# Kernel optimization log

Measured on AMD Instinct MI355X. Metric: run time of the kernel, lower is better.

## Reference

```python
import jax, jax.numpy as jnp
import numpy as np

B, N, D = 4096, 7, 512  # batch, sample_num, embed dim


def _l2_normalize(x, eps=1e-12):
    # torch F.normalize: x / max(||x||, eps)
    n = jnp.sqrt(jnp.sum(x * x, axis=-1, keepdims=True))
    return x / jnp.maximum(n, eps)


def setup_inputs() -> dict:
    key = jax.random.key(0)
    ks = jax.random.split(key, 6)
    return {
        "query_mean": jax.random.normal(ks[0], (B, D), jnp.float32),
        "query_logsigma": jax.random.normal(ks[1], (B, D), jnp.float32),
        "target_mean": jax.random.normal(ks[2], (B, D), jnp.float32),
        "target_logsigma": jax.random.normal(ks[3], (B, D), jnp.float32),
        "eps_q": jax.random.normal(ks[4], (B, N, D), jnp.float32),
        "eps_k": jax.random.normal(ks[5], (B, N, D), jnp.float32),
    }


def reference(query_mean, query_logsigma, target_mean, target_logsigma, eps_q, eps_k):
    temperature = 1.0
    qm = _l2_normalize(query_mean)               # [B, D]
    tm = _l2_normalize(target_mean)              # [B, D]
    # sample_gaussian_tensors: mu + eps * exp(logsigma), per-sample noise
    q = qm[:, None, :] + eps_q * jnp.exp(query_logsigma)[:, None, :]   # [B, N, D]
    k = tm[:, None, :] + eps_k * jnp.exp(target_logsigma)[:, None, :]  # [B, N, D]
    n = q.shape[1]
    # monto_carlo_estimation: score[i,j] = mean over N*N pairwise dots
    # = (sum_n q[i]) . (sum_m k[j]) / (N*N)  -- fused single gemm instead of B*B tiny matmuls
    score = jnp.einsum('id,jd->ij', q.sum(axis=1), k.sum(axis=1)) / (n * n)  # [B, B]
    logits = score / temperature
    # cross_entropy with labels = arange(B), reduction='mean'
    logp = jax.nn.log_softmax(logits, axis=-1)
    loss = -jnp.mean(jnp.diagonal(logp))
    return loss
```

## Files before the change

kernel.cpp:

```cpp
#include <hip/hip_runtime.h>

#define NBATCH 4096
#define NSAMP  7
#define DIM    512
#define NCB    16

typedef float floatx4 __attribute__((ext_vector_type(4)));
typedef short short8  __attribute__((ext_vector_type(8)));

__device__ static __forceinline__ void load16_lds(const void* g, void* l) {
  __builtin_amdgcn_global_load_lds(
      (const __attribute__((address_space(1))) unsigned int*)g,
      (__attribute__((address_space(3))) unsigned int*)l, 16, 0, 0);
}

__device__ static __forceinline__ unsigned int f2bf_rne(float f) {
  union { float f; unsigned int u; } v; v.f = f;
  unsigned int u = v.u;
  u += 0x7FFFu + ((u >> 16) & 1u);
  return u >> 16;
}

__global__ __launch_bounds__(256, 4) void prep_kernel(
    const float* __restrict__ qm, const float* __restrict__ qls, const float* __restrict__ eq,
    const float* __restrict__ tm, const float* __restrict__ tls, const float* __restrict__ ek,
    unsigned short* __restrict__ outA, unsigned short* __restrict__ outB)
{
  const int wv   = threadIdx.x >> 6;
  const int lane = threadIdx.x & 63;
  const int gid  = blockIdx.x * 4 + wv;
  const int side = gid >> 12;
  const int row  = gid & (NBATCH - 1);

  const float* mean = side ? tm  : qm;
  const float* ls   = side ? tls : qls;
  const float* eps  = side ? ek  : eq;
  unsigned short* out = side ? outB : outA;

  const float4* mean4 = (const float4*)(mean + (size_t)row * DIM);
  const float4* ls4   = (const float4*)(ls   + (size_t)row * DIM);
  const float4* eps4  = (const float4*)(eps  + (size_t)row * (NSAMP * DIM));

  const float4 m0 = mean4[lane];
  const float4 m1 = mean4[64 + lane];
  const float4 l0 = ls4[lane];
  const float4 l1 = ls4[64 + lane];
  float4 e0[NSAMP], e1[NSAMP];
  #pragma unroll
  for (int n = 0; n < NSAMP; ++n) {
    e0[n] = eps4[n * (DIM / 4) + lane];
    e1[n] = eps4[n * (DIM / 4) + 64 + lane];
  }

  float ss = m0.x * m0.x + m0.y * m0.y + m0.z * m0.z + m0.w * m0.w
           + m1.x * m1.x + m1.y * m1.y + m1.z * m1.z + m1.w * m1.w;
  #pragma unroll
  for (int off = 1; off < 64; off <<= 1) ss += __shfl_xor(ss, off);
  const float rnorm = 1.0f / fmaxf(sqrtf(ss), 1e-12f);

  float s00 = 0.f, s01 = 0.f, s02 = 0.f, s03 = 0.f;
  float s10 = 0.f, s11 = 0.f, s12 = 0.f, s13 = 0.f;
  #pragma unroll
  for (int n = 0; n < NSAMP; ++n) {
    s00 += e0[n].x; s01 += e0[n].y; s02 += e0[n].z; s03 += e0[n].w;
    s10 += e1[n].x; s11 += e1[n].y; s12 += e1[n].z; s13 += e1[n].w;
  }

  const float inv = 1.0f / (float)NSAMP;
  const float v00 = m0.x * rnorm + s00 * (__expf(l0.x) * inv);
  const float v01 = m0.y * rnorm + s01 * (__expf(l0.y) * inv);
  const float v02 = m0.z * rnorm + s02 * (__expf(l0.z) * inv);
  const float v03 = m0.w * rnorm + s03 * (__expf(l0.w) * inv);
  const float v10 = m1.x * rnorm + s10 * (__expf(l1.x) * inv);
  const float v11 = m1.y * rnorm + s11 * (__expf(l1.y) * inv);
  const float v12 = m1.z * rnorm + s12 * (__expf(l1.z) * inv);
  const float v13 = m1.w * rnorm + s13 * (__expf(l1.w) * inv);

  unsigned int* o32 = (unsigned int*)(out + (size_t)row * DIM);
  uint2 p0, p1;
  p0.x = f2bf_rne(v00) | (f2bf_rne(v01) << 16);
  p0.y = f2bf_rne(v02) | (f2bf_rne(v03) << 16);
  p1.x = f2bf_rne(v10) | (f2bf_rne(v11) << 16);
  p1.y = f2bf_rne(v12) | (f2bf_rne(v13) << 16);
  ((uint2*)o32)[lane] = p0;
  ((uint2*)(o32 + 128))[lane] = p1;
}


__device__ static __forceinline__ void stage_half(
    const unsigned short* __restrict__ Abf, const unsigned short* __restrict__ Bbf,
    int tileRow, int tileCol, int h, int kt, char* ldsbuf, int tid)
{
  const char* gsrc;
  if (h < 2) gsrc = (const char*)Abf + ((size_t)(tileRow * 256 + h * 128)) * (DIM * 2) + (size_t)kt * 128;
  else       gsrc = (const char*)Bbf + ((size_t)(tileCol * 256 + (h - 2) * 128)) * (DIM * 2) + (size_t)kt * 128;
  char* ldst = ldsbuf + h * 16384;
  #pragma unroll
  for (int q = 0; q < 2; ++q) {
    const int slot = q * 512 + tid;
    const int r    = slot >> 3;
    const int sc   = (slot & 7) ^ (r & 7);
    load16_lds(gsrc + (size_t)r * (DIM * 2) + sc * 16, ldst + slot * 16);
  }
}

__device__ static __forceinline__ short8 lds_frag(const char* base, int R, int c16) {
  return *(const short8*)(base + R * 128 + (((c16 ^ (R & 7)) << 4)));
}

__global__ __launch_bounds__(512) void gemm_lse_kernel(
    const unsigned short* __restrict__ Abf, const unsigned short* __restrict__ Bbf,
    float2* __restrict__ partial, float* __restrict__ diag)
{
  extern __shared__ char lds[];

  const int tid  = threadIdx.x;
  const int lane = tid & 63;
  const int wv   = tid >> 6;
  const int wm   = wv >> 2;
  const int wn   = wv & 3;
  const int fr   = lane & 15;
  const int kg   = lane >> 4;

  const int tileRow = blockIdx.y;
  const int tileCol = blockIdx.x;

  floatx4 acc[8][4];
  #pragma unroll
  for (int m = 0; m < 8; ++m)
    #pragma unroll
    for (int n = 0; n < 4; ++n)
      acc[m][n] = (floatx4){0.f, 0.f, 0.f, 0.f};

  #pragma unroll
  for (int h = 0; h < 4; ++h)
    stage_half(Abf, Bbf, tileRow, tileCol, h, 0, lds, tid);
  __syncthreads();

  short8 bb[4][2];
  for (int t = 0; t < 8; ++t) {
    const int ct = t & 1;
    const char* bA = lds + ct * 65536;
    const char* bB = bA + 32768;
    char* nbuf = lds + (ct ^ 1) * 65536;

    #pragma unroll
    for (int p = 0; p < 4; ++p) {
      if (t < 7) stage_half(Abf, Bbf, tileRow, tileCol, p, t + 1, nbuf, tid);

      const short8 a00 = lds_frag(bA, wm * 128 + (2 * p + 0) * 16 + fr, kg);
      const short8 a01 = lds_frag(bA, wm * 128 + (2 * p + 0) * 16 + fr, 4 + kg);
      const short8 a10 = lds_frag(bA, wm * 128 + (2 * p + 1) * 16 + fr, kg);
      const short8 a11 = lds_frag(bA, wm * 128 + (2 * p + 1) * 16 + fr, 4 + kg);
      if (p == 0) {
        #pragma unroll
        for (int n = 0; n < 4; ++n) {
          bb[n][0] = lds_frag(bB, wn * 64 + n * 16 + fr, kg);
          bb[n][1] = lds_frag(bB, wn * 64 + n * 16 + fr, 4 + kg);
        }
      }

      __builtin_amdgcn_s_barrier();
      __builtin_amdgcn_s_setprio(1);
      #pragma unroll
      for (int n = 0; n < 4; ++n) {
        acc[2 * p + 0][n] = __builtin_amdgcn_mfma_f32_16x16x32_bf16(a00, bb[n][0], acc[2 * p + 0][n], 0, 0, 0);
        acc[2 * p + 0][n] = __builtin_amdgcn_mfma_f32_16x16x32_bf16(a01, bb[n][1], acc[2 * p + 0][n], 0, 0, 0);
        acc[2 * p + 1][n] = __builtin_amdgcn_mfma_f32_16x16x32_bf16(a10, bb[n][0], acc[2 * p + 1][n], 0, 0, 0);
        acc[2 * p + 1][n] = __builtin_amdgcn_mfma_f32_16x16x32_bf16(a11, bb[n][1], acc[2 * p + 1][n], 0, 0, 0);
      }
      __builtin_amdgcn_s_setprio(0);
      __builtin_amdgcn_s_barrier();
    }
    __syncthreads();
  }

  float2* part = (float2*)lds;
  #pragma unroll
  for (int m = 0; m < 8; ++m) {
    #pragma unroll
    for (int rr = 0; rr < 4; ++rr) {
      const int lrow = wm * 128 + m * 16 + kg * 4 + rr;
      const int gi = tileRow * 256 + lrow;
      float lm = -3.0e38f;
      #pragma unroll
      for (int n = 0; n < 4; ++n) {
        const float c = acc[m][n][rr];
        const int gj = tileCol * 256 + wn * 64 + n * 16 + fr;
        if (gi == gj) diag[gi] = c;
        lm = fmaxf(lm, c);
      }
      #pragma unroll
      for (int off = 1; off < 16; off <<= 1) lm = fmaxf(lm, __shfl_xor(lm, off));
      float s = 0.f;
      #pragma unroll
      for (int n = 0; n < 4; ++n) s += __expf(acc[m][n][rr] - lm);
      #pragma unroll
      for (int off = 1; off < 16; off <<= 1) s += __shfl_xor(s, off);
      if (fr == 0) part[lrow * 4 + wn] = make_float2(lm, s);
    }
  }
  __syncthreads();
  if (tid < 256) {
    float2 p0 = part[tid * 4 + 0], p1 = part[tid * 4 + 1];
    float2 p2 = part[tid * 4 + 2], p3 = part[tid * 4 + 3];
    float M = fmaxf(fmaxf(p0.x, p1.x), fmaxf(p2.x, p3.x));
    float S = p0.y * __expf(p0.x - M) + p1.y * __expf(p1.x - M)
            + p2.y * __expf(p2.x - M) + p3.y * __expf(p3.x - M);
    partial[(size_t)(tileRow * 256 + tid) * NCB + tileCol] = make_float2(M, S);
  }
}

__global__ __launch_bounds__(256) void finalize1_kernel(
    const float2* __restrict__ partial, const float* __restrict__ diag,
    float* __restrict__ blocksum)
{
  const int i = blockIdx.x * 256 + threadIdx.x;
  const float2* p = partial + (size_t)i * NCB;
  float M = -3.0e38f;
  #pragma unroll
  for (int k = 0; k < NCB; ++k) M = fmaxf(M, p[k].x);
  float S = 0.f;
  #pragma unroll
  for (int k = 0; k < NCB; ++k) S += p[k].y * __expf(p[k].x - M);
  float v = M + logf(S) - diag[i];

  #pragma unroll
  for (int off = 1; off < 64; off <<= 1) v += __shfl_xor(v, off);
  __shared__ float wss[4];
  if ((threadIdx.x & 63) == 0) wss[threadIdx.x >> 6] = v;
  __syncthreads();
  if (threadIdx.x == 0)
    blocksum[blockIdx.x] = wss[0] + wss[1] + wss[2] + wss[3];
}

__global__ void finalize2_kernel(const float* __restrict__ blocksum, float* __restrict__ out)
{
  float s = 0.f;
  #pragma unroll
  for (int k = 0; k < 16; ++k) s += blocksum[k];
  out[0] = s * (1.0f / (float)NBATCH);
}

extern "C" void kernel_launch(void* const* d_in, const int* in_sizes, int n_in,
                              void* d_out, int out_size, void* d_ws, size_t ws_size,
                              hipStream_t stream) {
  const float* qm  = (const float*)d_in[0];
  const float* qls = (const float*)d_in[1];
  const float* tm  = (const float*)d_in[2];
  const float* tls = (const float*)d_in[3];
  const float* eq  = (const float*)d_in[4];
  const float* ek  = (const float*)d_in[5];
  float* out = (float*)d_out;

  char* ws = (char*)d_ws;
  unsigned short* Abf = (unsigned short*)ws;
  unsigned short* Bbf = (unsigned short*)(ws + (size_t)4194304);
  float2* partial = (float2*)(ws + (size_t)8388608);
  float*  diag    = (float*)(ws + (size_t)8388608 + 524288);
  float*  blocksum= (float*)(ws + (size_t)8388608 + 524288 + 16384);

  prep_kernel<<<dim3(NBATCH * 2 / 4), 256, 0, stream>>>(qm, qls, eq, tm, tls, ek, Abf, Bbf);
  gemm_lse_kernel<<<dim3(NCB, NCB), 512, 131072, stream>>>(Abf, Bbf, partial, diag);
  finalize1_kernel<<<NBATCH / 256, 256, 0, stream>>>(partial, diag, blocksum);
  finalize2_kernel<<<1, 1, 0, stream>>>(blocksum, out);
}
```

Baseline: 59.72 us.

## Stage eps loads via direct-to-LDS and fuse final reduction with ticket

The prep kernel now streams each row's eps samples straight into LDS with global_load_lds instead of holding 14 float4 registers per lane, and overlaps the exp of logsigma with those loads before a single vmcnt wait. The two finalize kernels are merged into one, where the last block to arrive (tracked by an atomic ticket reset in prep) sums the per-block partials, removing one kernel launch. The LDS use (56KB per block) and the launch-bounds change lower occupancy, and the ticket adds an atomic plus fences.

```diff
diff --git a/kernel.cpp b/kernel.cpp
--- a/kernel.cpp
+++ b/kernel.cpp
@@ -21,17 +21,22 @@
   return u >> 16;
 }
 
-__global__ __launch_bounds__(256, 4) void prep_kernel(
+__global__ __launch_bounds__(256, 2) void prep_kernel(
     const float* __restrict__ qm, const float* __restrict__ qls, const float* __restrict__ eq,
     const float* __restrict__ tm, const float* __restrict__ tls, const float* __restrict__ ek,
-    unsigned short* __restrict__ outA, unsigned short* __restrict__ outB)
-{
+    unsigned short* __restrict__ outA, unsigned short* __restrict__ outB,
+    unsigned int* __restrict__ ticket)
+{
+  __shared__ char seps[4][14336];
+
   const int wv   = threadIdx.x >> 6;
   const int lane = threadIdx.x & 63;
   const int gid  = blockIdx.x * 4 + wv;
   const int side = gid >> 12;
   const int row  = gid & (NBATCH - 1);
 
+  if (blockIdx.x == 0 && threadIdx.x == 0) *ticket = 0;
+
   const float* mean = side ? tm  : qm;
   const float* ls   = side ? tls : qls;
   const float* eps  = side ? ek  : eq;
@@ -39,42 +44,45 @@
 
   const float4* mean4 = (const float4*)(mean + (size_t)row * DIM);
   const float4* ls4   = (const float4*)(ls   + (size_t)row * DIM);
-  const float4* eps4  = (const float4*)(eps  + (size_t)row * (NSAMP * DIM));
+  const char* epsb = (const char*)(eps + (size_t)row * (NSAMP * DIM)) + lane * 16;
+  char* ldst = &seps[wv][0];
 
   const float4 m0 = mean4[lane];
   const float4 m1 = mean4[64 + lane];
   const float4 l0 = ls4[lane];
   const float4 l1 = ls4[64 + lane];
-  float4 e0[NSAMP], e1[NSAMP];
-  #pragma unroll
-  for (int n = 0; n < NSAMP; ++n) {
-    e0[n] = eps4[n * (DIM / 4) + lane];
-    e1[n] = eps4[n * (DIM / 4) + 64 + lane];
-  }
+  #pragma unroll
+  for (int c = 0; c < 14; ++c)
+    load16_lds(epsb + c * 1024, ldst + c * 1024);
 
   float ss = m0.x * m0.x + m0.y * m0.y + m0.z * m0.z + m0.w * m0.w
            + m1.x * m1.x + m1.y * m1.y + m1.z * m1.z + m1.w * m1.w;
   #pragma unroll
   for (int off = 1; off < 64; off <<= 1) ss += __shfl_xor(ss, off);
   const float rnorm = 1.0f / fmaxf(sqrtf(ss), 1e-12f);
-
-  float s00 = 0.f, s01 = 0.f, s02 = 0.f, s03 = 0.f;
-  float s10 = 0.f, s11 = 0.f, s12 = 0.f, s13 = 0.f;
+  const float inv = 1.0f / (float)NSAMP;
+  const float e00 = __expf(l0.x) * inv, e01 = __expf(l0.y) * inv;
+  const float e02 = __expf(l0.z) * inv, e03 = __expf(l0.w) * inv;
+  const float e10 = __expf(l1.x) * inv, e11 = __expf(l1.y) * inv;
+  const float e12 = __expf(l1.z) * inv, e13 = __expf(l1.w) * inv;
+
+  asm volatile("s_waitcnt vmcnt(0)" ::: "memory");
+  floatx4 a0 = (floatx4){0.f, 0.f, 0.f, 0.f};
+  floatx4 a1 = (floatx4){0.f, 0.f, 0.f, 0.f};
   #pragma unroll
   for (int n = 0; n < NSAMP; ++n) {
-    s00 += e0[n].x; s01 += e0[n].y; s02 += e0[n].z; s03 += e0[n].w;
-    s10 += e1[n].x; s11 += e1[n].y; s12 += e1[n].z; s13 += e1[n].w;
-  }
-
-  const float inv = 1.0f / (float)NSAMP;
-  const float v00 = m0.x * rnorm + s00 * (__expf(l0.x) * inv);
-  const float v01 = m0.y * rnorm + s01 * (__expf(l0.y) * inv);
-  const float v02 = m0.z * rnorm + s02 * (__expf(l0.z) * inv);
-  const float v03 = m0.w * rnorm + s03 * (__expf(l0.w) * inv);
-  const float v10 = m1.x * rnorm + s10 * (__expf(l1.x) * inv);
-  const float v11 = m1.y * rnorm + s11 * (__expf(l1.y) * inv);
-  const float v12 = m1.z * rnorm + s12 * (__expf(l1.z) * inv);
-  const float v13 = m1.w * rnorm + s13 * (__expf(l1.w) * inv);
+    a0 += *(const floatx4*)(ldst + (2 * n + 0) * 1024 + lane * 16);
+    a1 += *(const floatx4*)(ldst + (2 * n + 1) * 1024 + lane * 16);
+  }
+
+  const float v00 = m0.x * rnorm + a0[0] * e00;
+  const float v01 = m0.y * rnorm + a0[1] * e01;
+  const float v02 = m0.z * rnorm + a0[2] * e02;
+  const float v03 = m0.w * rnorm + a0[3] * e03;
+  const float v10 = m1.x * rnorm + a1[0] * e10;
+  const float v11 = m1.y * rnorm + a1[1] * e11;
+  const float v12 = m1.z * rnorm + a1[2] * e12;
+  const float v13 = m1.w * rnorm + a1[3] * e13;
 
   unsigned int* o32 = (unsigned int*)(out + (size_t)row * DIM);
   uint2 p0, p1;
@@ -211,9 +219,10 @@
   }
 }
 
-__global__ __launch_bounds__(256) void finalize1_kernel(
+__global__ __launch_bounds__(256) void finalize_kernel(
     const float2* __restrict__ partial, const float* __restrict__ diag,
-    float* __restrict__ blocksum)
+    float* __restrict__ blocksum, unsigned int* __restrict__ ticket,
+    float* __restrict__ out)
 {
   const int i = blockIdx.x * 256 + threadIdx.x;
   const float2* p = partial + (size_t)i * NCB;
@@ -228,18 +237,22 @@
   #pragma unroll
   for (int off = 1; off < 64; off <<= 1) v += __shfl_xor(v, off);
   __shared__ float wss[4];
+  __shared__ bool isLast;
   if ((threadIdx.x & 63) == 0) wss[threadIdx.x >> 6] = v;
   __syncthreads();
-  if (threadIdx.x == 0)
+  if (threadIdx.x == 0) {
     blocksum[blockIdx.x] = wss[0] + wss[1] + wss[2] + wss[3];
-}
-
-__global__ void finalize2_kernel(const float* __restrict__ blocksum, float* __restrict__ out)
-{
-  float s = 0.f;
-  #pragma unroll
-  for (int k = 0; k < 16; ++k) s += blocksum[k];
-  out[0] = s * (1.0f / (float)NBATCH);
+    __threadfence();
+    isLast = (atomicAdd(ticket, 1u) == 15u);
+  }
+  __syncthreads();
+  if (isLast && threadIdx.x == 0) {
+    __threadfence();
+    float s = 0.f;
+    #pragma unroll
+    for (int k = 0; k < 16; ++k) s += ((volatile float*)blocksum)[k];
+    out[0] = s * (1.0f / (float)NBATCH);
+  }
 }
 
 extern "C" void kernel_launch(void* const* d_in, const int* in_sizes, int n_in,
@@ -259,9 +272,9 @@
   float2* partial = (float2*)(ws + (size_t)8388608);
   float*  diag    = (float*)(ws + (size_t)8388608 + 524288);
   float*  blocksum= (float*)(ws + (size_t)8388608 + 524288 + 16384);
-
-  prep_kernel<<<dim3(NBATCH * 2 / 4), 256, 0, stream>>>(qm, qls, eq, tm, tls, ek, Abf, Bbf);
+  unsigned int* ticket = (unsigned int*)(ws + (size_t)8388608 + 524288 + 16384 + 64);
+
+  prep_kernel<<<dim3(NBATCH * 2 / 4), 256, 0, stream>>>(qm, qls, eq, tm, tls, ek, Abf, Bbf, ticket);
   gemm_lse_kernel<<<dim3(NCB, NCB), 512, 131072, stream>>>(Abf, Bbf, partial, diag);
-  finalize1_kernel<<<NBATCH / 256, 256, 0, stream>>>(partial, diag, blocksum);
-  finalize2_kernel<<<1, 1, 0, stream>>>(blocksum, out);
-}
+  finalize_kernel<<<NBATCH / 256, 256, 0, stream>>>(partial, diag, blocksum, ticket, out);
+}
```

Result: no change. 60.41 us (+1.2%).
